# Kernel optimization log

Measured on AMD Instinct MI355X. Metric: run time of the kernel, lower is better.

## Reference

```python
import jax, jax.numpy as jnp
import numpy as np

N_NODES = 20000
N_EDGES = 640000
F_IN = 128
HID = 128


def setup_inputs() -> dict:
    key = jax.random.key(0)
    ks = jax.random.split(key, 12)
    d = {}
    d["x"] = jax.random.normal(ks[0], (N_NODES, F_IN), dtype=jnp.float32)
    d["edge_index"] = jax.random.randint(ks[1], (2, N_EDGES), 0, N_NODES, dtype=jnp.int64)
    d["edge_weight"] = jax.random.uniform(ks[2], (N_EDGES,), dtype=jnp.float32)
    d["h"] = jax.random.normal(ks[3], (N_NODES, HID), dtype=jnp.float32)
    s1 = 1.0 / np.sqrt(F_IN)
    s2 = 1.0 / np.sqrt(HID)
    s3 = 1.0 / np.sqrt(2 * HID)
    d["W1"] = jax.random.uniform(ks[4], (F_IN, HID), jnp.float32, -s1, s1)
    d["b1"] = jnp.zeros((HID,), jnp.float32)
    d["W2"] = jax.random.uniform(ks[5], (HID, HID), jnp.float32, -s2, s2)
    d["b2"] = jnp.zeros((HID,), jnp.float32)
    d["Wu"] = jax.random.uniform(ks[6], (2 * HID, HID), jnp.float32, -s3, s3)
    d["bu"] = jax.random.uniform(ks[7], (HID,), jnp.float32, -s3, s3)
    d["Wr"] = jax.random.uniform(ks[8], (2 * HID, HID), jnp.float32, -s3, s3)
    d["br"] = jax.random.uniform(ks[9], (HID,), jnp.float32, -s3, s3)
    d["Wc"] = jax.random.uniform(ks[10], (2 * HID, HID), jnp.float32, -s3, s3)
    d["bc"] = jax.random.uniform(ks[11], (HID,), jnp.float32, -s3, s3)
    return d


def _gcn_layer(x, W, b, src, dst, norm, n):
    # GCNConv: transform then normalized scatter-add aggregation
    xw = x @ W                                    # [N, out]
    agg = jax.ops.segment_sum(xw[src] * norm[:, None], dst, num_segments=n)
    return agg + b


def reference(x, edge_index, edge_weight, h, W1, b1, W2, b2, Wu, bu, Wr, br, Wc, bc):
    n = x.shape[0]
    loops = jnp.arange(n, dtype=edge_index.dtype)
    src = jnp.concatenate([edge_index[0], loops])
    dst = jnp.concatenate([edge_index[1], loops])
    ew = jnp.concatenate([edge_weight, jnp.ones((n,), edge_weight.dtype)])
    # symmetric GCN normalization with self-loops
    deg = jax.ops.segment_sum(ew, dst, num_segments=n)
    dinv = jnp.where(deg > 0, jax.lax.rsqrt(deg), 0.0)
    norm = dinv[src] * ew * dinv[dst]             # [E+N]
    # 2-layer GCN: in->hid (ReLU) -> hid->hid
    h1 = jax.nn.relu(_gcn_layer(x, W1, b1, src, dst, norm, n))
    g = _gcn_layer(h1, W2, b2, src, dst, norm, n)
    xg = jax.nn.sigmoid(g)                        # [N, HID]
    # GRU-style gating
    xh = jnp.concatenate([xg, h], axis=-1)        # [N, 2*HID]
    u = jax.nn.sigmoid(xh @ Wu + bu)
    r = jax.nn.sigmoid(xh @ Wr + br)
    c = jnp.tanh(jnp.concatenate([xg, r * h], axis=-1) @ Wc + bc)
    return u * h + (1.0 - u) * c
```

## Files before the change

kernel.cpp:

```cpp
#include <hip/hip_runtime.h>
#include <math.h>

#define N_NODES 20000
#define N_EDGES 640000
#define HID 128
#define NPAD 20224
#define NBLK 79
#define NSHARD 8

typedef __attribute__((ext_vector_type(8))) short bf16x8;
typedef __attribute__((ext_vector_type(4))) float f32x4;

#define FIX_SCALE 274877906944.0
#define FIX_MASK ((1ull << 48) - 1)

__device__ inline short f2bf(float f) {
    unsigned u = __builtin_bit_cast(unsigned, f);
    u += 0x7fffu + ((u >> 16) & 1u);
    return (short)(u >> 16);
}
__device__ inline float bf2f(short s) {
    unsigned u = ((unsigned)(unsigned short)s) << 16;
    return __builtin_bit_cast(float, u);
}
__device__ inline float4 unpack_bf4(uint2 v) {
    float4 f;
    f.x = __builtin_bit_cast(float, v.x << 16);
    f.y = __builtin_bit_cast(float, v.x & 0xffff0000u);
    f.z = __builtin_bit_cast(float, v.y << 16);
    f.w = __builtin_bit_cast(float, v.y & 0xffff0000u);
    return f;
}
__device__ inline uint2 pack_bf4(float4 f) {
    uint2 v;
    v.x = (unsigned)(unsigned short)f2bf(f.x) | ((unsigned)(unsigned short)f2bf(f.y) << 16);
    v.y = (unsigned)(unsigned short)f2bf(f.z) | ((unsigned)(unsigned short)f2bf(f.w) << 16);
    return v;
}
__device__ inline bf16x8 cvt8(float4 a0, float4 a1) {
    bf16x8 v;
    v[0] = f2bf(a0.x); v[1] = f2bf(a0.y); v[2] = f2bf(a0.z); v[3] = f2bf(a0.w);
    v[4] = f2bf(a1.x); v[5] = f2bf(a1.y); v[6] = f2bf(a1.z); v[7] = f2bf(a1.w);
    return v;
}

__device__ inline float4 agg_node(int node, int half, int l,
                                  const short* __restrict__ xw,
                                  const int* __restrict__ rp,
                                  const int2* __restrict__ csr,
                                  const float* __restrict__ dinv) {
    float4 acc = {0.f, 0.f, 0.f, 0.f};
    if (half == 0) {
        float dv = dinv[node];
        float dv2 = dv * dv;
        float4 v = unpack_bf4(((const uint2*)(xw + (size_t)node * HID))[l]);
        acc.x = v.x * dv2; acc.y = v.y * dv2; acc.z = v.z * dv2; acc.w = v.w * dv2;
    }
    int j = rp[node], end = rp[node + 1];
    for (; j + 15 < end; j += 16) {
        int2 e[8];
#pragma unroll
        for (int i = 0; i < 8; i++) e[i] = csr[j + 2 * i + half];
        float4 v[8];
#pragma unroll
        for (int i = 0; i < 8; i++) v[i] = unpack_bf4(((const uint2*)(xw + (size_t)e[i].x * HID))[l]);
#pragma unroll
        for (int i = 0; i < 8; i++) {
            float w = __builtin_bit_cast(float, e[i].y);
            acc.x += v[i].x * w; acc.y += v[i].y * w; acc.z += v[i].z * w; acc.w += v[i].w * w;
        }
    }
    for (; j + 7 < end; j += 8) {
        int2 e[4];
#pragma unroll
        for (int i = 0; i < 4; i++) e[i] = csr[j + 2 * i + half];
        float4 v[4];
#pragma unroll
        for (int i = 0; i < 4; i++) v[i] = unpack_bf4(((const uint2*)(xw + (size_t)e[i].x * HID))[l]);
#pragma unroll
        for (int i = 0; i < 4; i++) {
            float w = __builtin_bit_cast(float, e[i].y);
            acc.x += v[i].x * w; acc.y += v[i].y * w; acc.z += v[i].z * w; acc.w += v[i].w * w;
        }
    }
    for (; j + 1 < end; j += 2) {
        int2 e0 = csr[j + half];
        float4 v0 = unpack_bf4(((const uint2*)(xw + (size_t)e0.x * HID))[l]);
        float w0 = __builtin_bit_cast(float, e0.y);
        acc.x += v0.x * w0; acc.y += v0.y * w0; acc.z += v0.z * w0; acc.w += v0.w * w0;
    }
    if (j < end && half == 0) {
        int2 e0 = csr[j];
        float4 v0 = unpack_bf4(((const uint2*)(xw + (size_t)e0.x * HID))[l]);
        float w0 = __builtin_bit_cast(float, e0.y);
        acc.x += v0.x * w0; acc.y += v0.y * w0; acc.z += v0.z * w0; acc.w += v0.w * w0;
    }
    acc.x += __shfl_xor(acc.x, 32);
    acc.y += __shfl_xor(acc.y, 32);
    acc.z += __shfl_xor(acc.z, 32);
    acc.w += __shfl_xor(acc.w, 32);
    return acc;
}

__global__ __launch_bounds__(256) void k_prep(const float* __restrict__ W1, const float* __restrict__ W2,
                                              const float* __restrict__ Wu, const float* __restrict__ Wr,
                                              const float* __restrict__ Wc,
                                              short* WT1, short* WT2, short* WTu, short* WTr, short* WTc,
                                              unsigned long long* packed) {
    int b = blockIdx.x;
    int tid = threadIdx.x;
    if (b < 512) {
        int i = b * 256 + tid;
        if (i < 32768) {
            const float* W = (i < 16384) ? W1 : W2;
            short* T = (i < 16384) ? WT1 : WT2;
            int j = i & 16383;
            int n = j >> 7, k = j & 127;
            T[n * 128 + k] = f2bf(W[k * 128 + n]);
        } else {
            int j = i - 32768;
            const float* W = Wu; short* T = WTu;
            if (j >= 65536)      { W = Wc; T = WTc; j -= 65536; }
            else if (j >= 32768) { W = Wr; T = WTr; j -= 32768; }
            int n = j >> 8, k = j & 255;
            T[n * 256 + k] = f2bf(W[k * 128 + n]);
        }
    } else {
        int i = (b - 512) * 256 + tid;
        if (i < NSHARD * NPAD) packed[i] = 0ull;
    }
}

__global__ __launch_bounds__(256) void k_hist_gemm(unsigned long long* packed, int* __restrict__ rank,
                                                   const int* __restrict__ dst,
                                                   const float* __restrict__ ew,
                                                   const float* __restrict__ x,
                                                   const short* __restrict__ WT1,
                                                   short* __restrict__ xw) {
    __shared__ short As[16 * 136];
    int tid = threadIdx.x;
    if (blockIdx.x < 2500) {
        int e = blockIdx.x * 256 + tid;
        int shard = blockIdx.x & (NSHARD - 1);
        int d = dst[e];
        unsigned long long add = (1ull << 48) | (unsigned long long)((double)ew[e] * FIX_SCALE);
        unsigned long long old = atomicAdd(&packed[shard * NPAD + d], add);
        rank[e] = (int)(old >> 48);
        return;
    }
    int r0 = (blockIdx.x - 2500) * 16;
    {
        int row = tid >> 4;
        int col0 = (tid & 15) * 8;
        const float* p = x + (size_t)(r0 + row) * HID + col0;
        *(bf16x8*)(&As[row * 136 + col0]) = cvt8(*(const float4*)p, *(const float4*)(p + 4));
    }
    __syncthreads();
    int wave = tid >> 6, lane = tid & 63;
    int m = lane & 15, quad = lane >> 4;
    f32x4 acc[2];
    acc[0] = (f32x4){0.f, 0.f, 0.f, 0.f};
    acc[1] = acc[0];
#pragma unroll
    for (int ks = 0; ks < 4; ks++) {
        int k0 = ks * 32 + quad * 8;
        bf16x8 a = *(const bf16x8*)(&As[m * 136 + k0]);
#pragma unroll
        for (int j = 0; j < 2; j++) {
            int n = (wave * 2 + j) * 16 + m;
            bf16x8 b = *(const bf16x8*)(WT1 + n * 128 + k0);
            acc[j] = __builtin_amdgcn_mfma_f32_16x16x32_bf16(a, b, acc[j], 0, 0, 0);
        }
    }
#pragma unroll
    for (int j = 0; j < 2; j++) {
        int col = (wave * 2 + j) * 16 + m;
#pragma unroll
        for (int rg = 0; rg < 4; rg++) {
            int grow = r0 + quad * 4 + rg;
            xw[(size_t)grow * HID + col] = f2bf(acc[j][rg]);
        }
    }
}

__global__ __launch_bounds__(256) void k_scan_part(const unsigned long long* __restrict__ packed,
                                                   int* __restrict__ tot, int* __restrict__ bsum) {
    __shared__ int red[256];
    int tid = threadIdx.x;
    int i = blockIdx.x * 256 + tid;
    int t = 0;
    if (i < N_NODES) {
#pragma unroll
        for (int s = 0; s < NSHARD; s++) t += (int)(packed[s * NPAD + i] >> 48);
        tot[i] = t;
    }
    red[tid] = t;
    __syncthreads();
    for (int off = 128; off > 0; off >>= 1) {
        if (tid < off) red[tid] += red[tid + off];
        __syncthreads();
    }
    if (tid == 0) bsum[blockIdx.x] = red[0];
}

__global__ __launch_bounds__(256) void k_scan_final(const unsigned long long* __restrict__ packed,
                                                    const int* __restrict__ tot,
                                                    const int* __restrict__ bsum,
                                                    int* __restrict__ rp, int* __restrict__ sb,
                                                    float* __restrict__ dinv) {
    __shared__ int smem[256];
    __shared__ int red[256];
    int tid = threadIdx.x;
    red[tid] = (tid < blockIdx.x) ? bsum[tid] : 0;
    int i = blockIdx.x * 256 + tid;
    int t = (i < N_NODES) ? tot[i] : 0;
    smem[tid] = t;
    __syncthreads();
    for (int off = 128; off > 0; off >>= 1) {
        if (tid < off) red[tid] += red[tid + off];
        __syncthreads();
    }
    for (int off = 1; off < 256; off <<= 1) {
        int x = (tid >= off) ? smem[tid - off] : 0;
        __syncthreads();
        smem[tid] += x;
        __syncthreads();
    }
    if (i < N_NODES) {
        int excl = smem[tid] - t + red[0];
        rp[i] = excl;
        if (i == N_NODES - 1) rp[N_NODES] = excl + t;
        int acc = excl;
        double deg = 1.0;
#pragma unroll
        for (int s = 0; s < NSHARD; s++) {
            unsigned long long p = packed[s * NPAD + i];
            sb[s * NPAD + i] = acc;
            acc += (int)(p >> 48);
            deg += (double)(p & FIX_MASK) * (1.0 / FIX_SCALE);
        }
        dinv[i] = rsqrtf((float)deg);
    }
}

__global__ __launch_bounds__(256) void k_fill(const int* __restrict__ src,
                                              const int* __restrict__ dst,
                                              const float* __restrict__ ew,
                                              const float* __restrict__ dinv,
                                              const int* __restrict__ sb,
                                              const int* __restrict__ rank,
                                              int2* __restrict__ csr) {
    int e = blockIdx.x * 256 + threadIdx.x;
    int shard = blockIdx.x & (NSHARD - 1);
    if (e < N_EDGES) {
        int s = src[e], d = dst[e];
        int slot = sb[shard * NPAD + d] + rank[e];
        float w = dinv[s] * ew[e] * dinv[d];
        csr[slot] = make_int2(s, __builtin_bit_cast(int, w));
    }
}

__global__ __launch_bounds__(256) void k_agg_gemm(const short* __restrict__ xw,
                                                  const int* __restrict__ rp,
                                                  const int2* __restrict__ csr,
                                                  const float* __restrict__ dinv,
                                                  const float* __restrict__ bias,
                                                  const short* __restrict__ WT2,
                                                  short* __restrict__ xw2) {
    __shared__ short As[16 * 136];
    int tid = threadIdx.x;
    int wave = tid >> 6, lane = tid & 63;
    int half = lane >> 5, l = lane & 31;
    int r0 = blockIdx.x * 16;
    float4 b = ((const float4*)bias)[l];
#pragma unroll
    for (int w = 0; w < 4; w++) {
        int trow = wave * 4 + w;
        float4 acc = agg_node(r0 + trow, half, l, xw, rp, csr, dinv);
        if (half == 0) {
            acc.x = fmaxf(acc.x + b.x, 0.f); acc.y = fmaxf(acc.y + b.y, 0.f);
            acc.z = fmaxf(acc.z + b.z, 0.f); acc.w = fmaxf(acc.w + b.w, 0.f);
            *(uint2*)(&As[trow * 136 + 4 * l]) = pack_bf4(acc);
        }
    }
    __syncthreads();
    int m = lane & 15, quad = lane >> 4;
    f32x4 acc[2];
    acc[0] = (f32x4){0.f, 0.f, 0.f, 0.f};
    acc[1] = acc[0];
#pragma unroll
    for (int ks = 0; ks < 4; ks++) {
        int k0 = ks * 32 + quad * 8;
        bf16x8 a = *(const bf16x8*)(&As[m * 136 + k0]);
#pragma unroll
        for (int j = 0; j < 2; j++) {
            int n = (wave * 2 + j) * 16 + m;
            bf16x8 bw = *(const bf16x8*)(WT2 + n * 128 + k0);
            acc[j] = __builtin_amdgcn_mfma_f32_16x16x32_bf16(a, bw, acc[j], 0, 0, 0);
        }
    }
#pragma unroll
    for (int j = 0; j < 2; j++) {
        int col = (wave * 2 + j) * 16 + m;
#pragma unroll
        for (int rg = 0; rg < 4; rg++) {
            int grow = r0 + quad * 4 + rg;
            xw2[(size_t)grow * HID + col] = f2bf(acc[j][rg]);
        }
    }
}

__global__ __launch_bounds__(256) void k_agg_gate(const short* __restrict__ xw2,
                                                  const int* __restrict__ rp,
                                                  const int2* __restrict__ csr,
                                                  const float* __restrict__ dinv,
                                                  const float* __restrict__ bias2,
                                                  const float* __restrict__ hf,
                                                  const short* __restrict__ WTu, const short* __restrict__ WTr,
                                                  const short* __restrict__ WTc,
                                                  const float* __restrict__ pbu, const float* __restrict__ pbr,
                                                  const float* __restrict__ pbc,
                                                  float* __restrict__ out) {
    __shared__ short Xs[16 * 264];
    int tid = threadIdx.x;
    int wave = tid >> 6, lane = tid & 63;
    int half = lane >> 5, l = lane & 31;
    int r0 = blockIdx.x * 16;
    {
        int row = tid >> 4;
        int col0 = (tid & 15) * 8;
        const float* p = hf + (size_t)(r0 + row) * HID + col0;
        *(bf16x8*)(&Xs[row * 264 + 128 + col0]) = cvt8(*(const float4*)p, *(const float4*)(p + 4));
    }
    float4 b2 = ((const float4*)bias2)[l];
#pragma unroll
    for (int w = 0; w < 4; w++) {
        int trow = wave * 4 + w;
        float4 acc = agg_node(r0 + trow, half, l, xw2, rp, csr, dinv);
        if (half == 0) {
            acc.x = 1.f / (1.f + __expf(-(acc.x + b2.x)));
            acc.y = 1.f / (1.f + __expf(-(acc.y + b2.y)));
            acc.z = 1.f / (1.f + __expf(-(acc.z + b2.z)));
            acc.w = 1.f / (1.f + __expf(-(acc.w + b2.w)));
            *(uint2*)(&Xs[trow * 264 + 4 * l]) = pack_bf4(acc);
        }
    }
    __syncthreads();
    int m = lane & 15, quad = lane >> 4;
    f32x4 au[2], ar[2];
    au[0] = (f32x4){0.f, 0.f, 0.f, 0.f};
    au[1] = au[0]; ar[0] = au[0]; ar[1] = au[0];
#pragma unroll
    for (int ks = 0; ks < 8; ks++) {
        int k0 = ks * 32 + quad * 8;
        bf16x8 a = *(const bf16x8*)(&Xs[m * 264 + k0]);
#pragma unroll
        for (int j = 0; j < 2; j++) {
            int n = (wave * 2 + j) * 16 + m;
            bf16x8 bu_f = *(const bf16x8*)(WTu + n * 256 + k0);
            au[j] = __builtin_amdgcn_mfma_f32_16x16x32_bf16(a, bu_f, au[j], 0, 0, 0);
            bf16x8 br_f = *(const bf16x8*)(WTr + n * 256 + k0);
            ar[j] = __builtin_amdgcn_mfma_f32_16x16x32_bf16(a, br_f, ar[j], 0, 0, 0);
        }
    }
    __syncthreads();
#pragma unroll
    for (int j = 0; j < 2; j++) {
        int col = (wave * 2 + j) * 16 + m;
        float brv = pbr[col];
#pragma unroll
        for (int rg = 0; rg < 4; rg++) {
            int trow = quad * 4 + rg;
            float rv = 1.f / (1.f + __expf(-(ar[j][rg] + brv)));
            float hv = bf2f(Xs[trow * 264 + 128 + col]);
            Xs[trow * 264 + 128 + col] = f2bf(rv * hv);
        }
    }
    __syncthreads();
    f32x4 ac[2];
    ac[0] = (f32x4){0.f, 0.f, 0.f, 0.f};
    ac[1] = ac[0];
#pragma unroll
    for (int ks = 0; ks < 8; ks++) {
        int k0 = ks * 32 + quad * 8;
        bf16x8 a = *(const bf16x8*)(&Xs[m * 264 + k0]);
#pragma unroll
        for (int j = 0; j < 2; j++) {
            int n = (wave * 2 + j) * 16 + m;
            bf16x8 bc_f = *(const bf16x8*)(WTc + n * 256 + k0);
            ac[j] = __builtin_amdgcn_mfma_f32_16x16x32_bf16(a, bc_f, ac[j], 0, 0, 0);
        }
    }
#pragma unroll
    for (int j = 0; j < 2; j++) {
        int col = (wave * 2 + j) * 16 + m;
        float buv = pbu[col], bcv = pbc[col];
#pragma unroll
        for (int rg = 0; rg < 4; rg++) {
            int grow = r0 + quad * 4 + rg;
            float uv = 1.f / (1.f + __expf(-(au[j][rg] + buv)));
            float cv = tanhf(ac[j][rg] + bcv);
            float hv = hf[(size_t)grow * HID + col];
            out[(size_t)grow * HID + col] = uv * hv + (1.f - uv) * cv;
        }
    }
}

extern "C" void kernel_launch(void* const* d_in, const int* in_sizes, int n_in,
                              void* d_out, int out_size, void* d_ws, size_t ws_size,
                              hipStream_t stream) {
    const float* x  = (const float*)d_in[0];
    const int*   ei = (const int*)d_in[1];
    const float* ew = (const float*)d_in[2];
    const float* h  = (const float*)d_in[3];
    const float* W1 = (const float*)d_in[4];
    const float* b1 = (const float*)d_in[5];
    const float* W2 = (const float*)d_in[6];
    const float* b2 = (const float*)d_in[7];
    const float* Wu = (const float*)d_in[8];
    const float* bu = (const float*)d_in[9];
    const float* Wr = (const float*)d_in[10];
    const float* br = (const float*)d_in[11];
    const float* Wc = (const float*)d_in[12];
    const float* bc = (const float*)d_in[13];
    const int* src = ei;
    const int* dst = ei + N_EDGES;
    float* out = (float*)d_out;

    const size_t NH = (size_t)N_NODES * HID;
    float* ws = (float*)d_ws;
    float* dinv = ws;
    int*   rp   = (int*)(ws + NPAD);
    unsigned long long* packed = (unsigned long long*)(ws + 2 * NPAD);
    int*   sb   = (int*)(ws + 18 * NPAD);
    int*   tot  = (int*)(ws + 26 * NPAD);
    int*   bsum = (int*)(ws + 27 * NPAD);
    int*   rank = (int*)(ws + 27 * NPAD + 128);
    int2*  csr  = (int2*)(ws + 27 * NPAD + 128 + N_EDGES);
    short* xw   = (short*)(ws + 27 * NPAD + 128 + 3 * N_EDGES);
    short* xw2  = xw + NH;
    short* WT1 = xw2 + NH;
    short* WT2 = WT1 + 16384;
    short* WTu = WT2 + 16384;
    short* WTr = WTu + 32768;
    short* WTc = WTr + 32768;

    k_prep<<<512 + (NSHARD * NPAD + 255) / 256, 256, 0, stream>>>(
        W1, W2, Wu, Wr, Wc, WT1, WT2, WTu, WTr, WTc, packed);
    k_hist_gemm<<<2500 + N_NODES / 16, 256, 0, stream>>>(packed, rank, dst, ew, x, WT1, xw);
    k_scan_part<<<NBLK, 256, 0, stream>>>(packed, tot, bsum);
    k_scan_final<<<NBLK, 256, 0, stream>>>(packed, tot, bsum, rp, sb, dinv);
    k_fill<<<N_EDGES / 256, 256, 0, stream>>>(src, dst, ew, dinv, sb, rank, csr);
    k_agg_gemm<<<N_NODES / 16, 256, 0, stream>>>(xw, rp, csr, dinv, b1, WT2, xw2);
    k_agg_gate<<<N_NODES / 16, 256, 0, stream>>>(xw2, rp, csr, dinv, b2, h,
                                                 WTu, WTr, WTc, bu, br, bc, out);
}
```

Before: 255.4 us.

## Use 1024-thread blocks with one wave per node in aggregation kernels

The two aggregation+GEMM kernels now launch 16 waves per block, so each wave aggregates one node instead of four nodes in sequence. This exposes more parallelism for the latency-bound gather. The MFMA work is re-split: 8 waves compute the layer-2 transform, and in the gate kernel waves 0-7 compute the u gate while waves 8-15 compute r, then waves 0-7 compute c. The cost is larger blocks that may limit occupancy and leave half the waves idle during the GEMM phases.

```diff
diff --git a/kernel.cpp b/kernel.cpp
--- a/kernel.cpp
+++ b/kernel.cpp
@@ -260,146 +260,121 @@
     }
 }
 
-__global__ __launch_bounds__(256) void k_agg_gemm(const short* __restrict__ xw,
-                                                  const int* __restrict__ rp,
-                                                  const int2* __restrict__ csr,
-                                                  const float* __restrict__ dinv,
-                                                  const float* __restrict__ bias,
-                                                  const short* __restrict__ WT2,
-                                                  short* __restrict__ xw2) {
+__global__ __launch_bounds__(1024) void k_agg_gemm(const short* __restrict__ xw,
+                                                   const int* __restrict__ rp,
+                                                   const int2* __restrict__ csr,
+                                                   const float* __restrict__ dinv,
+                                                   const float* __restrict__ bias,
+                                                   const short* __restrict__ WT2,
+                                                   short* __restrict__ xw2) {
     __shared__ short As[16 * 136];
-    int tid = threadIdx.x;
-    int wave = tid >> 6, lane = tid & 63;
-    int half = lane >> 5, l = lane & 31;
-    int r0 = blockIdx.x * 16;
-    float4 b = ((const float4*)bias)[l];
-#pragma unroll
-    for (int w = 0; w < 4; w++) {
-        int trow = wave * 4 + w;
-        float4 acc = agg_node(r0 + trow, half, l, xw, rp, csr, dinv);
-        if (half == 0) {
-            acc.x = fmaxf(acc.x + b.x, 0.f); acc.y = fmaxf(acc.y + b.y, 0.f);
-            acc.z = fmaxf(acc.z + b.z, 0.f); acc.w = fmaxf(acc.w + b.w, 0.f);
-            *(uint2*)(&As[trow * 136 + 4 * l]) = pack_bf4(acc);
-        }
-    }
-    __syncthreads();
-    int m = lane & 15, quad = lane >> 4;
-    f32x4 acc[2];
-    acc[0] = (f32x4){0.f, 0.f, 0.f, 0.f};
-    acc[1] = acc[0];
-#pragma unroll
-    for (int ks = 0; ks < 4; ks++) {
-        int k0 = ks * 32 + quad * 8;
-        bf16x8 a = *(const bf16x8*)(&As[m * 136 + k0]);
-#pragma unroll
-        for (int j = 0; j < 2; j++) {
-            int n = (wave * 2 + j) * 16 + m;
-            bf16x8 bw = *(const bf16x8*)(WT2 + n * 128 + k0);
-            acc[j] = __builtin_amdgcn_mfma_f32_16x16x32_bf16(a, bw, acc[j], 0, 0, 0);
-        }
-    }
-#pragma unroll
-    for (int j = 0; j < 2; j++) {
-        int col = (wave * 2 + j) * 16 + m;
-#pragma unroll
-        for (int rg = 0; rg < 4; rg++) {
-            int grow = r0 + quad * 4 + rg;
-            xw2[(size_t)grow * HID + col] = f2bf(acc[j][rg]);
-        }
-    }
-}
-
-__global__ __launch_bounds__(256) void k_agg_gate(const short* __restrict__ xw2,
-                                                  const int* __restrict__ rp,
-                                                  const int2* __restrict__ csr,
-                                                  const float* __restrict__ dinv,
-                                                  const float* __restrict__ bias2,
-                                                  const float* __restrict__ hf,
-                                                  const short* __restrict__ WTu, const short* __restrict__ WTr,
-                                                  const short* __restrict__ WTc,
-                                                  const float* __restrict__ pbu, const float* __restrict__ pbr,
-                                                  const float* __restrict__ pbc,
-                                                  float* __restrict__ out) {
-    __shared__ short Xs[16 * 264];
     int tid = threadIdx.x;
     int wave = tid >> 6, lane = tid & 63;
     int half = lane >> 5, l = lane & 31;
     int r0 = blockIdx.x * 16;
     {
+        float4 b = ((const float4*)bias)[l];
+        float4 acc = agg_node(r0 + wave, half, l, xw, rp, csr, dinv);
+        if (half == 0) {
+            acc.x = fmaxf(acc.x + b.x, 0.f); acc.y = fmaxf(acc.y + b.y, 0.f);
+            acc.z = fmaxf(acc.z + b.z, 0.f); acc.w = fmaxf(acc.w + b.w, 0.f);
+            *(uint2*)(&As[wave * 136 + 4 * l]) = pack_bf4(acc);
+        }
+    }
+    __syncthreads();
+    if (wave < 8) {
+        int m = lane & 15, quad = lane >> 4;
+        f32x4 acc = (f32x4){0.f, 0.f, 0.f, 0.f};
+#pragma unroll
+        for (int ks = 0; ks < 4; ks++) {
+            int k0 = ks * 32 + quad * 8;
+            bf16x8 a = *(const bf16x8*)(&As[m * 136 + k0]);
+            bf16x8 b = *(const bf16x8*)(WT2 + (wave * 16 + m) * 128 + k0);
+            acc = __builtin_amdgcn_mfma_f32_16x16x32_bf16(a, b, acc, 0, 0, 0);
+        }
+        int col = wave * 16 + m;
+#pragma unroll
+        for (int rg = 0; rg < 4; rg++) {
+            int grow = r0 + quad * 4 + rg;
+            xw2[(size_t)grow * HID + col] = f2bf(acc[rg]);
+        }
+    }
+}
+
+__global__ __launch_bounds__(1024) void k_agg_gate(const short* __restrict__ xw2,
+                                                   const int* __restrict__ rp,
+                                                   const int2* __restrict__ csr,
+                                                   const float* __restrict__ dinv,
+                                                   const float* __restrict__ bias2,
+                                                   const float* __restrict__ hf,
+                                                   const short* __restrict__ WTu, const short* __restrict__ WTr,
+                                                   const short* __restrict__ WTc,
+                                                   const float* __restrict__ pbu, const float* __restrict__ pbr,
+                                                   const float* __restrict__ pbc,
+                                                   float* __restrict__ out) {
+    __shared__ short Xs[16 * 264];
+    int tid = threadIdx.x;
+    int wave = tid >> 6, lane = tid & 63;
+    int half = lane >> 5, l = lane & 31;
+    int r0 = blockIdx.x * 16;
+    if (tid < 256) {
         int row = tid >> 4;
         int col0 = (tid & 15) * 8;
         const float* p = hf + (size_t)(r0 + row) * HID + col0;
         *(bf16x8*)(&Xs[row * 264 + 128 + col0]) = cvt8(*(const float4*)p, *(const float4*)(p + 4));
     }
-    float4 b2 = ((const float4*)bias2)[l];
-#pragma unroll
-    for (int w = 0; w < 4; w++) {
-        int trow = wave * 4 + w;
-        float4 acc = agg_node(r0 + trow, half, l, xw2, rp, csr, dinv);
+    {
+        float4 b2 = ((const float4*)bias2)[l];
+        float4 acc = agg_node(r0 + wave, half, l, xw2, rp, csr, dinv);
         if (half == 0) {
             acc.x = 1.f / (1.f + __expf(-(acc.x + b2.x)));
             acc.y = 1.f / (1.f + __expf(-(acc.y + b2.y)));
             acc.z = 1.f / (1.f + __expf(-(acc.z + b2.z)));
             acc.w = 1.f / (1.f + __expf(-(acc.w + b2.w)));
-            *(uint2*)(&Xs[trow * 264 + 4 * l]) = pack_bf4(acc);
+            *(uint2*)(&Xs[wave * 264 + 4 * l]) = pack_bf4(acc);
         }
     }
     __syncthreads();
     int m = lane & 15, quad = lane >> 4;
-    f32x4 au[2], ar[2];
-    au[0] = (f32x4){0.f, 0.f, 0.f, 0.f};
-    au[1] = au[0]; ar[0] = au[0]; ar[1] = au[0];
+    int t = wave & 7;
+    const short* WTur = (wave < 8) ? WTu : WTr;
+    f32x4 a_ur = (f32x4){0.f, 0.f, 0.f, 0.f};
 #pragma unroll
     for (int ks = 0; ks < 8; ks++) {
         int k0 = ks * 32 + quad * 8;
         bf16x8 a = *(const bf16x8*)(&Xs[m * 264 + k0]);
-#pragma unroll
-        for (int j = 0; j < 2; j++) {
-            int n = (wave * 2 + j) * 16 + m;
-            bf16x8 bu_f = *(const bf16x8*)(WTu + n * 256 + k0);
-            au[j] = __builtin_amdgcn_mfma_f32_16x16x32_bf16(a, bu_f, au[j], 0, 0, 0);
-            bf16x8 br_f = *(const bf16x8*)(WTr + n * 256 + k0);
-            ar[j] = __builtin_amdgcn_mfma_f32_16x16x32_bf16(a, br_f, ar[j], 0, 0, 0);
-        }
-    }
-    __syncthreads();
-#pragma unroll
-    for (int j = 0; j < 2; j++) {
-        int col = (wave * 2 + j) * 16 + m;
+        bf16x8 b = *(const bf16x8*)(WTur + (t * 16 + m) * 256 + k0);
+        a_ur = __builtin_amdgcn_mfma_f32_16x16x32_bf16(a, b, a_ur, 0, 0, 0);
+    }
+    __syncthreads();
+    if (wave >= 8) {
+        int col = t * 16 + m;
         float brv = pbr[col];
 #pragma unroll
         for (int rg = 0; rg < 4; rg++) {
             int trow = quad * 4 + rg;
-            float rv = 1.f / (1.f + __expf(-(ar[j][rg] + brv)));
+            float rv = 1.f / (1.f + __expf(-(a_ur[rg] + brv)));
             float hv = bf2f(Xs[trow * 264 + 128 + col]);
             Xs[trow * 264 + 128 + col] = f2bf(rv * hv);
         }
     }
     __syncthreads();
-    f32x4 ac[2];
-    ac[0] = (f32x4){0.f, 0.f, 0.f, 0.f};
-    ac[1] = ac[0];
-#pragma unroll
-    for (int ks = 0; ks < 8; ks++) {
-        int k0 = ks * 32 + quad * 8;
-        bf16x8 a = *(const bf16x8*)(&Xs[m * 264 + k0]);
-#pragma unroll
-        for (int j = 0; j < 2; j++) {
-            int n = (wave * 2 + j) * 16 + m;
-            bf16x8 bc_f = *(const bf16x8*)(WTc + n * 256 + k0);
-            ac[j] = __builtin_amdgcn_mfma_f32_16x16x32_bf16(a, bc_f, ac[j], 0, 0, 0);
-        }
-    }
-#pragma unroll
-    for (int j = 0; j < 2; j++) {
-        int col = (wave * 2 + j) * 16 + m;
+    if (wave < 8) {
+        f32x4 ac = (f32x4){0.f, 0.f, 0.f, 0.f};
+#pragma unroll
+        for (int ks = 0; ks < 8; ks++) {
+            int k0 = ks * 32 + quad * 8;
+            bf16x8 a = *(const bf16x8*)(&Xs[m * 264 + k0]);
+            bf16x8 b = *(const bf16x8*)(WTc + (t * 16 + m) * 256 + k0);
+            ac = __builtin_amdgcn_mfma_f32_16x16x32_bf16(a, b, ac, 0, 0, 0);
+        }
+        int col = t * 16 + m;
         float buv = pbu[col], bcv = pbc[col];
 #pragma unroll
         for (int rg = 0; rg < 4; rg++) {
             int grow = r0 + quad * 4 + rg;
-            float uv = 1.f / (1.f + __expf(-(au[j][rg] + buv)));
-            float cv = tanhf(ac[j][rg] + bcv);
+            float uv = 1.f / (1.f + __expf(-(a_ur[rg] + buv)));
+            float cv = tanhf(ac[rg] + bcv);
             float hv = hf[(size_t)grow * HID + col];
             out[(size_t)grow * HID + col] = uv * hv + (1.f - uv) * cv;
         }
@@ -451,7 +426,7 @@
     k_scan_part<<<NBLK, 256, 0, stream>>>(packed, tot, bsum);
     k_scan_final<<<NBLK, 256, 0, stream>>>(packed, tot, bsum, rp, sb, dinv);
     k_fill<<<N_EDGES / 256, 256, 0, stream>>>(src, dst, ew, dinv, sb, rank, csr);
-    k_agg_gemm<<<N_NODES / 16, 256, 0, stream>>>(xw, rp, csr, dinv, b1, WT2, xw2);
-    k_agg_gate<<<N_NODES / 16, 256, 0, stream>>>(xw2, rp, csr, dinv, b2, h,
-                                                 WTu, WTr, WTc, bu, br, bc, out);
-}
+    k_agg_gemm<<<N_NODES / 16, 1024, 0, stream>>>(xw, rp, csr, dinv, b1, WT2, xw2);
+    k_agg_gate<<<N_NODES / 16, 1024, 0, stream>>>(xw2, rp, csr, dinv, b2, h,
+                                                  WTu, WTr, WTc, bu, br, bc, out);
+}
```

Result: no change. 256.7 us (+0.5%).

## Store transformed features in fp8 and split aggregation from GEMM kernels

Applied to the files above, without the earlier changes.

The XW intermediates that are gathered per edge are now stored as fp8 instead of bf16, halving the bytes read in the sparse gather. The fused aggregate+GEMM kernels are split into a standalone aggregation kernel (one wave per node, finer grid) followed by separate GEMM/gate kernels, with bf16 intermediates for the aggregated outputs. This trades precision loss from fp8 and extra kernel launches and intermediate round-trips for less gather traffic and better load balance.

```diff
diff --git a/kernel.cpp b/kernel.cpp
--- a/kernel.cpp
+++ b/kernel.cpp
@@ -10,6 +10,7 @@
 
 typedef __attribute__((ext_vector_type(8))) short bf16x8;
 typedef __attribute__((ext_vector_type(4))) float f32x4;
+typedef __attribute__((ext_vector_type(2))) float f32x2;
 
 #define FIX_SCALE 274877906944.0
 #define FIX_MASK ((1ull << 48) - 1)
@@ -22,14 +23,6 @@
 __device__ inline float bf2f(short s) {
     unsigned u = ((unsigned)(unsigned short)s) << 16;
     return __builtin_bit_cast(float, u);
-}
-__device__ inline float4 unpack_bf4(uint2 v) {
-    float4 f;
-    f.x = __builtin_bit_cast(float, v.x << 16);
-    f.y = __builtin_bit_cast(float, v.x & 0xffff0000u);
-    f.z = __builtin_bit_cast(float, v.y << 16);
-    f.w = __builtin_bit_cast(float, v.y & 0xffff0000u);
-    return f;
 }
 __device__ inline uint2 pack_bf4(float4 f) {
     uint2 v;
@@ -43,9 +36,17 @@
     v[4] = f2bf(a1.x); v[5] = f2bf(a1.y); v[6] = f2bf(a1.z); v[7] = f2bf(a1.w);
     return v;
 }
+__device__ inline unsigned char f2fp8(float f) {
+    return (unsigned char)(__builtin_amdgcn_cvt_pk_fp8_f32(f, f, 0, false) & 0xff);
+}
+__device__ inline float4 unpack_fp8x4(unsigned v) {
+    f32x2 lo = __builtin_amdgcn_cvt_pk_f32_fp8((int)v, false);
+    f32x2 hi = __builtin_amdgcn_cvt_pk_f32_fp8((int)v, true);
+    return make_float4(lo[0], lo[1], hi[0], hi[1]);
+}
 
 __device__ inline float4 agg_node(int node, int half, int l,
-                                  const short* __restrict__ xw,
+                                  const unsigned char* __restrict__ xw,
                                   const int* __restrict__ rp,
                                   const int2* __restrict__ csr,
                                   const float* __restrict__ dinv) {
@@ -53,7 +54,7 @@
     if (half == 0) {
         float dv = dinv[node];
         float dv2 = dv * dv;
-        float4 v = unpack_bf4(((const uint2*)(xw + (size_t)node * HID))[l]);
+        float4 v = unpack_fp8x4(((const unsigned*)(xw + (size_t)node * HID))[l]);
         acc.x = v.x * dv2; acc.y = v.y * dv2; acc.z = v.z * dv2; acc.w = v.w * dv2;
     }
     int j = rp[node], end = rp[node + 1];
@@ -61,39 +62,41 @@
         int2 e[8];
 #pragma unroll
         for (int i = 0; i < 8; i++) e[i] = csr[j + 2 * i + half];
-        float4 v[8];
-#pragma unroll
-        for (int i = 0; i < 8; i++) v[i] = unpack_bf4(((const uint2*)(xw + (size_t)e[i].x * HID))[l]);
+        unsigned v[8];
+#pragma unroll
+        for (int i = 0; i < 8; i++) v[i] = ((const unsigned*)(xw + (size_t)e[i].x * HID))[l];
 #pragma unroll
         for (int i = 0; i < 8; i++) {
             float w = __builtin_bit_cast(float, e[i].y);
-            acc.x += v[i].x * w; acc.y += v[i].y * w; acc.z += v[i].z * w; acc.w += v[i].w * w;
+            float4 f = unpack_fp8x4(v[i]);
+            acc.x += f.x * w; acc.y += f.y * w; acc.z += f.z * w; acc.w += f.w * w;
         }
     }
     for (; j + 7 < end; j += 8) {
         int2 e[4];
 #pragma unroll
         for (int i = 0; i < 4; i++) e[i] = csr[j + 2 * i + half];
-        float4 v[4];
-#pragma unroll
-        for (int i = 0; i < 4; i++) v[i] = unpack_bf4(((const uint2*)(xw + (size_t)e[i].x * HID))[l]);
+        unsigned v[4];
+#pragma unroll
+        for (int i = 0; i < 4; i++) v[i] = ((const unsigned*)(xw + (size_t)e[i].x * HID))[l];
 #pragma unroll
         for (int i = 0; i < 4; i++) {
             float w = __builtin_bit_cast(float, e[i].y);
-            acc.x += v[i].x * w; acc.y += v[i].y * w; acc.z += v[i].z * w; acc.w += v[i].w * w;
+            float4 f = unpack_fp8x4(v[i]);
+            acc.x += f.x * w; acc.y += f.y * w; acc.z += f.z * w; acc.w += f.w * w;
         }
     }
     for (; j + 1 < end; j += 2) {
         int2 e0 = csr[j + half];
-        float4 v0 = unpack_bf4(((const uint2*)(xw + (size_t)e0.x * HID))[l]);
+        float4 f = unpack_fp8x4(((const unsigned*)(xw + (size_t)e0.x * HID))[l]);
         float w0 = __builtin_bit_cast(float, e0.y);
-        acc.x += v0.x * w0; acc.y += v0.y * w0; acc.z += v0.z * w0; acc.w += v0.w * w0;
+        acc.x += f.x * w0; acc.y += f.y * w0; acc.z += f.z * w0; acc.w += f.w * w0;
     }
     if (j < end && half == 0) {
         int2 e0 = csr[j];
-        float4 v0 = unpack_bf4(((const uint2*)(xw + (size_t)e0.x * HID))[l]);
+        float4 f = unpack_fp8x4(((const unsigned*)(xw + (size_t)e0.x * HID))[l]);
         float w0 = __builtin_bit_cast(float, e0.y);
-        acc.x += v0.x * w0; acc.y += v0.y * w0; acc.z += v0.z * w0; acc.w += v0.w * w0;
+        acc.x += f.x * w0; acc.y += f.y * w0; acc.z += f.z * w0; acc.w += f.w * w0;
     }
     acc.x += __shfl_xor(acc.x, 32);
     acc.y += __shfl_xor(acc.y, 32);
@@ -136,7 +139,7 @@
                                                    const float* __restrict__ ew,
                                                    const float* __restrict__ x,
                                                    const short* __restrict__ WT1,
-                                                   short* __restrict__ xw) {
+                                                   unsigned char* __restrict__ xw) {
     __shared__ short As[16 * 136];
     int tid = threadIdx.x;
     if (blockIdx.x < 2500) {
@@ -178,7 +181,7 @@
 #pragma unroll
         for (int rg = 0; rg < 4; rg++) {
             int grow = r0 + quad * 4 + rg;
-            xw[(size_t)grow * HID + col] = f2bf(acc[j][rg]);
+            xw[(size_t)grow * HID + col] = f2fp8(acc[j][rg]);
         }
     }
 }
@@ -260,30 +263,44 @@
     }
 }
 
-__global__ __launch_bounds__(256) void k_agg_gemm(const short* __restrict__ xw,
-                                                  const int* __restrict__ rp,
-                                                  const int2* __restrict__ csr,
-                                                  const float* __restrict__ dinv,
-                                                  const float* __restrict__ bias,
-                                                  const short* __restrict__ WT2,
-                                                  short* __restrict__ xw2) {
+__global__ __launch_bounds__(256) void k_agg(const unsigned char* __restrict__ xw,
+                                             short* __restrict__ outb,
+                                             const int* __restrict__ rp,
+                                             const int2* __restrict__ csr,
+                                             const float* __restrict__ dinv,
+                                             const float* __restrict__ bias,
+                                             int act) {
+    int node = blockIdx.x * 4 + (threadIdx.x >> 6);
+    int lane = threadIdx.x & 63;
+    int half = lane >> 5, l = lane & 31;
+    float4 acc = agg_node(node, half, l, xw, rp, csr, dinv);
+    if (half == 0) {
+        float4 b = ((const float4*)bias)[l];
+        acc.x += b.x; acc.y += b.y; acc.z += b.z; acc.w += b.w;
+        if (act == 0) {
+            acc.x = fmaxf(acc.x, 0.f); acc.y = fmaxf(acc.y, 0.f);
+            acc.z = fmaxf(acc.z, 0.f); acc.w = fmaxf(acc.w, 0.f);
+        } else {
+            acc.x = 1.f / (1.f + __expf(-acc.x)); acc.y = 1.f / (1.f + __expf(-acc.y));
+            acc.z = 1.f / (1.f + __expf(-acc.z)); acc.w = 1.f / (1.f + __expf(-acc.w));
+        }
+        ((uint2*)(outb + (size_t)node * HID))[l] = pack_bf4(acc);
+    }
+}
+
+__global__ __launch_bounds__(256) void k_gemm2(const short* __restrict__ Ab,
+                                               const short* __restrict__ WT,
+                                               unsigned char* __restrict__ Cb) {
     __shared__ short As[16 * 136];
     int tid = threadIdx.x;
+    int r0 = blockIdx.x * 16;
+    {
+        int row = tid >> 4;
+        int col0 = (tid & 15) * 8;
+        *(bf16x8*)(&As[row * 136 + col0]) = *(const bf16x8*)(Ab + (size_t)(r0 + row) * HID + col0);
+    }
+    __syncthreads();
     int wave = tid >> 6, lane = tid & 63;
-    int half = lane >> 5, l = lane & 31;
-    int r0 = blockIdx.x * 16;
-    float4 b = ((const float4*)bias)[l];
-#pragma unroll
-    for (int w = 0; w < 4; w++) {
-        int trow = wave * 4 + w;
-        float4 acc = agg_node(r0 + trow, half, l, xw, rp, csr, dinv);
-        if (half == 0) {
-            acc.x = fmaxf(acc.x + b.x, 0.f); acc.y = fmaxf(acc.y + b.y, 0.f);
-            acc.z = fmaxf(acc.z + b.z, 0.f); acc.w = fmaxf(acc.w + b.w, 0.f);
-            *(uint2*)(&As[trow * 136 + 4 * l]) = pack_bf4(acc);
-        }
-    }
-    __syncthreads();
     int m = lane & 15, quad = lane >> 4;
     f32x4 acc[2];
     acc[0] = (f32x4){0.f, 0.f, 0.f, 0.f};
@@ -295,8 +312,8 @@
 #pragma unroll
         for (int j = 0; j < 2; j++) {
             int n = (wave * 2 + j) * 16 + m;
-            bf16x8 bw = *(const bf16x8*)(WT2 + n * 128 + k0);
-            acc[j] = __builtin_amdgcn_mfma_f32_16x16x32_bf16(a, bw, acc[j], 0, 0, 0);
+            bf16x8 b = *(const bf16x8*)(WT + n * 128 + k0);
+            acc[j] = __builtin_amdgcn_mfma_f32_16x16x32_bf16(a, b, acc[j], 0, 0, 0);
         }
     }
 #pragma unroll
@@ -305,47 +322,38 @@
 #pragma unroll
         for (int rg = 0; rg < 4; rg++) {
             int grow = r0 + quad * 4 + rg;
-            xw2[(size_t)grow * HID + col] = f2bf(acc[j][rg]);
-        }
-    }
-}
-
-__global__ __launch_bounds__(256) void k_agg_gate(const short* __restrict__ xw2,
-                                                  const int* __restrict__ rp,
-                                                  const int2* __restrict__ csr,
-                                                  const float* __restrict__ dinv,
-                                                  const float* __restrict__ bias2,
-                                                  const float* __restrict__ hf,
-                                                  const short* __restrict__ WTu, const short* __restrict__ WTr,
-                                                  const short* __restrict__ WTc,
-                                                  const float* __restrict__ pbu, const float* __restrict__ pbr,
-                                                  const float* __restrict__ pbc,
-                                                  float* __restrict__ out) {
+            Cb[(size_t)grow * HID + col] = f2fp8(acc[j][rg]);
+        }
+    }
+}
+
+__global__ __launch_bounds__(256) void k_gate(const short* __restrict__ xgb,
+                                              const float* __restrict__ hf,
+                                              const short* __restrict__ WTu, const short* __restrict__ WTr,
+                                              const short* __restrict__ WTc,
+                                              const float* __restrict__ pbu, const float* __restrict__ pbr,
+                                              const float* __restrict__ pbc,
+                                              float* __restrict__ out) {
     __shared__ short Xs[16 * 264];
     int tid = threadIdx.x;
+    int r0 = blockIdx.x * 16;
+#pragma unroll
+    for (int i = 0; i < 2; i++) {
+        int c = tid + i * 256;
+        int row = c >> 5;
+        int col0 = (c & 31) * 8;
+        int grow = r0 + row;
+        bf16x8 v;
+        if (col0 < 128) {
+            v = *(const bf16x8*)(xgb + (size_t)grow * HID + col0);
+        } else {
+            const float* p = hf + (size_t)grow * HID + (col0 - 128);
+            v = cvt8(*(const float4*)p, *(const float4*)(p + 4));
+        }
+        *(bf16x8*)(&Xs[row * 264 + col0]) = v;
+    }
+    __syncthreads();
     int wave = tid >> 6, lane = tid & 63;
-    int half = lane >> 5, l = lane & 31;
-    int r0 = blockIdx.x * 16;
-    {
-        int row = tid >> 4;
-        int col0 = (tid & 15) * 8;
-        const float* p = hf + (size_t)(r0 + row) * HID + col0;
-        *(bf16x8*)(&Xs[row * 264 + 128 + col0]) = cvt8(*(const float4*)p, *(const float4*)(p + 4));
-    }
-    float4 b2 = ((const float4*)bias2)[l];
-#pragma unroll
-    for (int w = 0; w < 4; w++) {
-        int trow = wave * 4 + w;
-        float4 acc = agg_node(r0 + trow, half, l, xw2, rp, csr, dinv);
-        if (half == 0) {
-            acc.x = 1.f / (1.f + __expf(-(acc.x + b2.x)));
-            acc.y = 1.f / (1.f + __expf(-(acc.y + b2.y)));
-            acc.z = 1.f / (1.f + __expf(-(acc.z + b2.z)));
-            acc.w = 1.f / (1.f + __expf(-(acc.w + b2.w)));
-            *(uint2*)(&Xs[trow * 264 + 4 * l]) = pack_bf4(acc);
-        }
-    }
-    __syncthreads();
     int m = lane & 15, quad = lane >> 4;
     f32x4 au[2], ar[2];
     au[0] = (f32x4){0.f, 0.f, 0.f, 0.f};
@@ -437,9 +445,11 @@
     int*   bsum = (int*)(ws + 27 * NPAD);
     int*   rank = (int*)(ws + 27 * NPAD + 128);
     int2*  csr  = (int2*)(ws + 27 * NPAD + 128 + N_EDGES);
-    short* xw   = (short*)(ws + 27 * NPAD + 128 + 3 * N_EDGES);
-    short* xw2  = xw + NH;
-    short* WT1 = xw2 + NH;
+    unsigned char* xw  = (unsigned char*)(ws + 27 * NPAD + 128 + 3 * N_EDGES);
+    unsigned char* xw2 = xw + NH;
+    short* h1b = (short*)(xw2 + NH);
+    short* xgb = h1b + NH;
+    short* WT1 = xgb + NH;
     short* WT2 = WT1 + 16384;
     short* WTu = WT2 + 16384;
     short* WTr = WTu + 32768;
@@ -451,7 +461,8 @@
     k_scan_part<<<NBLK, 256, 0, stream>>>(packed, tot, bsum);
     k_scan_final<<<NBLK, 256, 0, stream>>>(packed, tot, bsum, rp, sb, dinv);
     k_fill<<<N_EDGES / 256, 256, 0, stream>>>(src, dst, ew, dinv, sb, rank, csr);
-    k_agg_gemm<<<N_NODES / 16, 256, 0, stream>>>(xw, rp, csr, dinv, b1, WT2, xw2);
-    k_agg_gate<<<N_NODES / 16, 256, 0, stream>>>(xw2, rp, csr, dinv, b2, h,
-                                                 WTu, WTr, WTc, bu, br, bc, out);
-}
+    k_agg<<<N_NODES / 4, 256, 0, stream>>>(xw, h1b, rp, csr, dinv, b1, 0);
+    k_gemm2<<<N_NODES / 16, 256, 0, stream>>>(h1b, WT2, xw2);
+    k_agg<<<N_NODES / 4, 256, 0, stream>>>(xw2, xgb, rp, csr, dinv, b2, 1);
+    k_gate<<<N_NODES / 16, 256, 0, stream>>>(xgb, h, WTu, WTr, WTc, bu, br, bc, out);
+}
```

Result: faster. 230.0 us (-9.9%).
